# Optimization experiments

Hardware: AMD Instinct MI355X
Metric: run time of the kernel (lower is better)

## Reference

```python
import jax, jax.numpy as jnp
import numpy as np

THRESHOLD = 0.5


def setup_inputs() -> dict:
    key = jax.random.key(0)
    T, B = 2048, 4096
    x = jax.random.uniform(key, (T, B, 2), dtype=jnp.float32)  # push/pop signals in [0,1]
    state0 = jnp.zeros((B, 2), dtype=jnp.float32)  # [count, tanh(count)]
    return {"x": x, "state0": state0}


def _step(state, xt):
    # state: [B, 2] = [count, tanh(count)]; xt: [B, 2] = [push, pop]
    push_sig = xt[..., 0]
    pop_sig = xt[..., 1]
    is_push = (push_sig >= THRESHOLD) & (push_sig >= pop_sig)
    is_pop = (pop_sig >= THRESHOLD) & (pop_sig > push_sig)
    delta = jnp.where(is_push, 1.0, jnp.where(is_pop, -1.0, 0.0))
    count = state[..., 0] + delta
    new_state = jnp.stack([count, jnp.tanh(count)], axis=-1)
    return new_state, new_state


def reference(x, state0):
    # x: [T, B, 2], state0: [B, 2] -> all per-step states [T, B, 2]
    _, states = jax.lax.scan(_step, state0, x)
    return states
```

## Files before the change

kernel.cpp:

```cpp
#include <hip/hip_runtime.h>
#include <math.h>

#define T_TOTAL 2048
#define B_TOTAL 4096
#define B2      (B_TOTAL / 2)
#define NCHUNK  64
#define TCHUNK  (T_TOTAL / NCHUNK)

__device__ __forceinline__ int delta_of(float p, float q) {
    return (p >= 0.5f && p >= q) ? 1 : ((q >= 0.5f && q > p) ? -1 : 0);
}

__device__ __forceinline__ float fast_tanh(float x) {
    float e = __builtin_amdgcn_exp2f(x * 2.885390081777927f);
    return 1.0f - 2.0f / (e + 1.0f);
}

__global__ void scan_pass1(const float* __restrict__ x,
                           int* __restrict__ partial,
                           ulonglong2* __restrict__ packed) {
    const int p = blockIdx.x * blockDim.x + threadIdx.x;
    const int c = blockIdx.y;
    const float4* __restrict__ x4 = (const float4*)x;
    const int t0 = c * TCHUNK;

    int s0 = 0, s1 = 0;
    unsigned long long w0 = 0ull, w1 = 0ull;

#pragma unroll
    for (int t = 0; t < 16; ++t) {
        float4 v = x4[(size_t)(t0 + t) * B2 + p];
        int d0 = delta_of(v.x, v.y);
        int d1 = delta_of(v.z, v.w);
        s0 += d0; s1 += d1;
        unsigned int nib = (unsigned int)(d0 & 3) | ((unsigned int)(d1 & 3) << 2);
        w0 |= (unsigned long long)nib << (4 * t);
    }
#pragma unroll
    for (int t = 16; t < 32; ++t) {
        float4 v = x4[(size_t)(t0 + t) * B2 + p];
        int d0 = delta_of(v.x, v.y);
        int d1 = delta_of(v.z, v.w);
        s0 += d0; s1 += d1;
        unsigned int nib = (unsigned int)(d0 & 3) | ((unsigned int)(d1 & 3) << 2);
        w1 |= (unsigned long long)nib << (4 * (t - 16));
    }

    ulonglong2 w; w.x = w0; w.y = w1;
    packed[(size_t)c * B2 + p] = w;
    int2 s; s.x = s0; s.y = s1;
    ((int2*)partial)[(size_t)c * B2 + p] = s;
}

__global__ void scan_pass2(int* __restrict__ partial) {
    const int b = blockIdx.x * blockDim.x + threadIdx.x;
    int off = 0;
#pragma unroll
    for (int c = 0; c < NCHUNK; ++c) {
        int v = partial[(size_t)c * B_TOTAL + b];
        partial[(size_t)c * B_TOTAL + b] = off;
        off += v;
    }
}

__device__ __forceinline__ int sext2(unsigned int bits2) {
    return ((int)(bits2 << 30)) >> 30;
}

__global__ void scan_pass3(const int* __restrict__ partial,
                           const ulonglong2* __restrict__ packed,
                           float* __restrict__ out) {
    const int p = blockIdx.x * blockDim.x + threadIdx.x;
    const int c = blockIdx.y;
    float4* __restrict__ o4 = (float4*)out;
    const int t0 = c * TCHUNK;

    int2 pr = ((const int2*)partial)[(size_t)c * B2 + p];
    int c0 = pr.x, c1 = pr.y;
    ulonglong2 w = packed[(size_t)c * B2 + p];

#pragma unroll
    for (int t = 0; t < 16; ++t) {
        unsigned int nib = (unsigned int)(w.x >> (4 * t)) & 0xFu;
        c0 += sext2(nib & 3u);
        c1 += sext2(nib >> 2);
        float f0 = (float)c0, f1 = (float)c1;
        float4 o; o.x = f0; o.y = fast_tanh(f0); o.z = f1; o.w = fast_tanh(f1);
        o4[(size_t)(t0 + t) * B2 + p] = o;
    }
#pragma unroll
    for (int t = 16; t < 32; ++t) {
        unsigned int nib = (unsigned int)(w.y >> (4 * (t - 16))) & 0xFu;
        c0 += sext2(nib & 3u);
        c1 += sext2(nib >> 2);
        float f0 = (float)c0, f1 = (float)c1;
        float4 o; o.x = f0; o.y = fast_tanh(f0); o.z = f1; o.w = fast_tanh(f1);
        o4[(size_t)(t0 + t) * B2 + p] = o;
    }
}

__global__ void naive_scan(const float* __restrict__ x, float* __restrict__ out) {
    const int b = blockIdx.x * blockDim.x + threadIdx.x;
    if (b >= B_TOTAL) return;
    const float2* __restrict__ x2 = (const float2*)x;
    float2* __restrict__ o2 = (float2*)out;
    int count = 0;
    for (int t = 0; t < T_TOTAL; ++t) {
        float2 v = x2[(size_t)t * B_TOTAL + b];
        count += delta_of(v.x, v.y);
        float fc = (float)count;
        float2 w; w.x = fc; w.y = tanhf(fc);
        o2[(size_t)t * B_TOTAL + b] = w;
    }
}

extern "C" void kernel_launch(void* const* d_in, const int* in_sizes, int n_in,
                              void* d_out, int out_size, void* d_ws, size_t ws_size,
                              hipStream_t stream) {
    const float* x = (const float*)d_in[0];
    float* out = (float*)d_out;

    const size_t partial_bytes = (size_t)NCHUNK * B_TOTAL * sizeof(int);
    const size_t packed_bytes  = (size_t)NCHUNK * B2 * sizeof(ulonglong2);
    if (ws_size < partial_bytes + packed_bytes) {
        naive_scan<<<dim3((B_TOTAL + 255) / 256), dim3(256), 0, stream>>>(x, out);
        return;
    }
    int* partial = (int*)d_ws;
    ulonglong2* packed = (ulonglong2*)((char*)d_ws + partial_bytes);

    dim3 block(256);
    dim3 grid1(B2 / 256, NCHUNK);
    scan_pass1<<<grid1, block, 0, stream>>>(x, partial, packed);
    scan_pass2<<<dim3(B_TOTAL / 256), block, 0, stream>>>(partial);
    scan_pass3<<<grid1, block, 0, stream>>>(partial, packed, out);
}
```

Before: 115.5 us.

## Fold chunk-offset scan into emit kernel and use nontemporal loads/stores

Removes the separate pass that scanned per-chunk partial sums. Each emit thread now sums the partials of all earlier chunks itself, which saves one kernel launch and the read-modify-write of the partial buffer. In exchange, later chunks do up to 63 redundant serial loads each. Input loads and output stores are also marked nontemporal to reduce cache pollution on the streaming traffic.

```diff
diff --git a/kernel.cpp b/kernel.cpp
--- a/kernel.cpp
+++ b/kernel.cpp
@@ -6,6 +6,8 @@
 #define B2      (B_TOTAL / 2)
 #define NCHUNK  64
 #define TCHUNK  (T_TOTAL / NCHUNK)
+
+typedef float fvec4 __attribute__((ext_vector_type(4)));
 
 __device__ __forceinline__ int delta_of(float p, float q) {
     return (p >= 0.5f && p >= q) ? 1 : ((q >= 0.5f && q > p) ? -1 : 0);
@@ -16,12 +18,16 @@
     return 1.0f - 2.0f / (e + 1.0f);
 }
 
-__global__ void scan_pass1(const float* __restrict__ x,
-                           int* __restrict__ partial,
-                           ulonglong2* __restrict__ packed) {
+__device__ __forceinline__ int sext2(unsigned int bits2) {
+    return ((int)(bits2 << 30)) >> 30;
+}
+
+__global__ void __launch_bounds__(256)
+scan_pass1(const fvec4* __restrict__ x4,
+           int2* __restrict__ partial,
+           ulonglong2* __restrict__ packed) {
     const int p = blockIdx.x * blockDim.x + threadIdx.x;
     const int c = blockIdx.y;
-    const float4* __restrict__ x4 = (const float4*)x;
     const int t0 = c * TCHUNK;
 
     int s0 = 0, s1 = 0;
@@ -29,7 +35,7 @@
 
 #pragma unroll
     for (int t = 0; t < 16; ++t) {
-        float4 v = x4[(size_t)(t0 + t) * B2 + p];
+        fvec4 v = __builtin_nontemporal_load(&x4[(size_t)(t0 + t) * B2 + p]);
         int d0 = delta_of(v.x, v.y);
         int d1 = delta_of(v.z, v.w);
         s0 += d0; s1 += d1;
@@ -38,7 +44,7 @@
     }
 #pragma unroll
     for (int t = 16; t < 32; ++t) {
-        float4 v = x4[(size_t)(t0 + t) * B2 + p];
+        fvec4 v = __builtin_nontemporal_load(&x4[(size_t)(t0 + t) * B2 + p]);
         int d0 = delta_of(v.x, v.y);
         int d1 = delta_of(v.z, v.w);
         s0 += d0; s1 += d1;
@@ -49,34 +55,23 @@
     ulonglong2 w; w.x = w0; w.y = w1;
     packed[(size_t)c * B2 + p] = w;
     int2 s; s.x = s0; s.y = s1;
-    ((int2*)partial)[(size_t)c * B2 + p] = s;
+    partial[(size_t)c * B2 + p] = s;
 }
 
-__global__ void scan_pass2(int* __restrict__ partial) {
-    const int b = blockIdx.x * blockDim.x + threadIdx.x;
-    int off = 0;
-#pragma unroll
-    for (int c = 0; c < NCHUNK; ++c) {
-        int v = partial[(size_t)c * B_TOTAL + b];
-        partial[(size_t)c * B_TOTAL + b] = off;
-        off += v;
-    }
-}
-
-__device__ __forceinline__ int sext2(unsigned int bits2) {
-    return ((int)(bits2 << 30)) >> 30;
-}
-
-__global__ void scan_pass3(const int* __restrict__ partial,
-                           const ulonglong2* __restrict__ packed,
-                           float* __restrict__ out) {
+__global__ void __launch_bounds__(256)
+scan_emit(const int2* __restrict__ partial,
+          const ulonglong2* __restrict__ packed,
+          fvec4* __restrict__ o4) {
     const int p = blockIdx.x * blockDim.x + threadIdx.x;
     const int c = blockIdx.y;
-    float4* __restrict__ o4 = (float4*)out;
     const int t0 = c * TCHUNK;
 
-    int2 pr = ((const int2*)partial)[(size_t)c * B2 + p];
-    int c0 = pr.x, c1 = pr.y;
+    int c0 = 0, c1 = 0;
+    for (int cc = 0; cc < c; ++cc) {
+        int2 v = partial[(size_t)cc * B2 + p];
+        c0 += v.x; c1 += v.y;
+    }
+
     ulonglong2 w = packed[(size_t)c * B2 + p];
 
 #pragma unroll
@@ -85,8 +80,8 @@
         c0 += sext2(nib & 3u);
         c1 += sext2(nib >> 2);
         float f0 = (float)c0, f1 = (float)c1;
-        float4 o; o.x = f0; o.y = fast_tanh(f0); o.z = f1; o.w = fast_tanh(f1);
-        o4[(size_t)(t0 + t) * B2 + p] = o;
+        fvec4 o; o.x = f0; o.y = fast_tanh(f0); o.z = f1; o.w = fast_tanh(f1);
+        __builtin_nontemporal_store(o, &o4[(size_t)(t0 + t) * B2 + p]);
     }
 #pragma unroll
     for (int t = 16; t < 32; ++t) {
@@ -94,8 +89,8 @@
         c0 += sext2(nib & 3u);
         c1 += sext2(nib >> 2);
         float f0 = (float)c0, f1 = (float)c1;
-        float4 o; o.x = f0; o.y = fast_tanh(f0); o.z = f1; o.w = fast_tanh(f1);
-        o4[(size_t)(t0 + t) * B2 + p] = o;
+        fvec4 o; o.x = f0; o.y = fast_tanh(f0); o.z = f1; o.w = fast_tanh(f1);
+        __builtin_nontemporal_store(o, &o4[(size_t)(t0 + t) * B2 + p]);
     }
 }
 
@@ -120,18 +115,17 @@
     const float* x = (const float*)d_in[0];
     float* out = (float*)d_out;
 
-    const size_t partial_bytes = (size_t)NCHUNK * B_TOTAL * sizeof(int);
+    const size_t partial_bytes = (size_t)NCHUNK * B2 * sizeof(int2);
     const size_t packed_bytes  = (size_t)NCHUNK * B2 * sizeof(ulonglong2);
     if (ws_size < partial_bytes + packed_bytes) {
         naive_scan<<<dim3((B_TOTAL + 255) / 256), dim3(256), 0, stream>>>(x, out);
         return;
     }
-    int* partial = (int*)d_ws;
+    int2* partial = (int2*)d_ws;
     ulonglong2* packed = (ulonglong2*)((char*)d_ws + partial_bytes);
 
     dim3 block(256);
-    dim3 grid1(B2 / 256, NCHUNK);
-    scan_pass1<<<grid1, block, 0, stream>>>(x, partial, packed);
-    scan_pass2<<<dim3(B_TOTAL / 256), block, 0, stream>>>(partial);
-    scan_pass3<<<grid1, block, 0, stream>>>(partial, packed, out);
+    dim3 grid(B2 / 256, NCHUNK);
+    scan_pass1<<<grid, block, 0, stream>>>((const fvec4*)x, partial, packed);
+    scan_emit<<<grid, block, 0, stream>>>(partial, packed, (fvec4*)out);
 }
```

Result: slower. 118.5 us (+2.7%).
